# Optimization experiments

Hardware: AMD Instinct MI355X
Metric: run time of the kernel (lower is better)

Reference implementation:

```python
import jax, jax.numpy as jnp
import numpy as np

D_MODEL = 1024
D_K = 1024
D_V = 1024


def setup_inputs() -> dict:
    key = jax.random.key(0)
    kx, kq, kk, kv = jax.random.split(key, 4)
    B, T = 4, 2048
    x = jax.random.normal(kx, (B, T, D_MODEL), dtype=jnp.float32)
    # nn.Linear(d_model, d_k, bias=False) weight has shape (d_k, d_model); y = x @ W.T
    s = 1.0 / np.sqrt(D_MODEL)
    Wq = jax.random.uniform(kq, (D_K, D_MODEL), jnp.float32, -s, s)
    Wk = jax.random.uniform(kk, (D_K, D_MODEL), jnp.float32, -s, s)
    Wv = jax.random.uniform(kv, (D_V, D_MODEL), jnp.float32, -s, s)
    return {"x": x, "Wq": Wq, "Wk": Wk, "Wv": Wv}


def reference(x, Wq, Wk, Wv):
    # x: [B, T, D]; W*: [d_out, D]
    Q = jnp.einsum('btd,kd->btk', x, Wq)  # [B, T, d_k]
    K = jnp.einsum('btd,kd->btk', x, Wk)  # [B, T, d_k]
    V = jnp.einsum('btd,vd->btv', x, Wv)  # [B, T, d_v]
    scores = jnp.einsum('btk,bsk->bts', Q, K) / jnp.sqrt(jnp.float32(D_K))
    attn = jax.nn.softmax(scores, axis=-1)
    out = jnp.einsum('bts,bsv->btv', attn, V)  # [B, T, d_v]
    return out
```

## Files before the change

kernel.cpp:

```cpp
#include <hip/hip_runtime.h>
#include <hip/hip_bf16.h>
#include <stdint.h>

#define TT     2048
#define DMODEL 1024
#define NBATCH 4

typedef __bf16 bf16x8 __attribute__((ext_vector_type(8)));
typedef __bf16 bf16x4 __attribute__((ext_vector_type(4)));
typedef float  f32x4  __attribute__((ext_vector_type(4)));

#define GPTR(p) ((const __attribute__((address_space(1))) void*)(p))
#define LPTR(p) ((__attribute__((address_space(3))) void*)(p))

__global__ __launch_bounds__(256) void cvt_all(
    const float* __restrict__ x,  const float* __restrict__ wq,
    const float* __restrict__ wk, const float* __restrict__ wv,
    __bf16* __restrict__ xb,  __bf16* __restrict__ wqb,
    __bf16* __restrict__ wkb, __bf16* __restrict__ wvb,
    int nx4, int nw4)
{
    int i = blockIdx.x * 256 + threadIdx.x;
    const float* src; __bf16* dst; int off;
    if (i < nx4)                { src = x;  dst = xb;  off = i; }
    else if (i < nx4 + nw4)     { src = wq; dst = wqb; off = i - nx4; }
    else if (i < nx4 + 2 * nw4) { src = wk; dst = wkb; off = i - nx4 - nw4; }
    else if (i < nx4 + 3 * nw4) { src = wv; dst = wvb; off = i - nx4 - 2 * nw4; }
    else return;
    float4 v = ((const float4*)src)[off];
    bf16x4 o;
    o[0] = (__bf16)v.x; o[1] = (__bf16)v.y; o[2] = (__bf16)v.z; o[3] = (__bf16)v.w;
    ((bf16x4*)dst)[off] = o;
}

template <typename OutT, int BN, int WRN, bool YMAJOR, int MODE>
__global__ __launch_bounds__(512, 2) void gemm256(
    const __bf16* __restrict__ A, const __bf16* __restrict__ B,
    OutT* __restrict__ C, float* __restrict__ Rw, int N, int Kd,
    long sA, long sB, long sC, float scale)
{
    constexpr int WCN  = 8 / WRN;
    constexpr int WM   = 256 / WRN;
    constexpr int WN   = BN / WCN;
    constexpr int IW   = WM / 16;
    constexpr int IH   = IW / 2;
    constexpr int JW   = WN / 16;
    constexpr int JH   = JW / 2;
    constexpr int QB   = BN / 64;
    constexpr int BSTR = BN * 128;

    __shared__ __align__(16) char lds[65536 + 2 * BSTR];

    const int nx = gridDim.x, ny = gridDim.y;
    const int fid = blockIdx.x + nx * (blockIdx.y + ny * blockIdx.z);
    const int chunk = (nx * ny * gridDim.z) >> 3;
    const int g = (fid & 7) * chunk + (fid >> 3);
    int bx, by, bz;
    if (YMAJOR) { by = g % ny; int r = g / ny; bx = r % nx; bz = r / nx; }
    else        { bx = g % nx; int r = g / nx; by = r % ny; bz = r / ny; }

    A += (size_t)bz * (size_t)sA;
    B += (size_t)bz * (size_t)sB;
    C += (size_t)bz * (size_t)sC;

    const int tid  = threadIdx.x;
    const int lane = tid & 63;
    const int wid  = tid >> 6;
    const int wr   = wid / WCN;
    const int wc   = wid % WCN;
    const int kg   = lane >> 4;
    const int rl   = lane & 15;

    const int m0 = bx * 256;
    const int n0 = by * BN;

    const int swzX   = (rl & 7) << 4;
    const int lo0    = ((0 << 6) | (kg << 4)) ^ swzX;
    const int lo1    = ((1 << 6) | (kg << 4)) ^ swzX;
    const int baseA  = wr * (WM * 128) + rl * 128;
    const int baseBr = wc * (WN * 128) + rl * 128;

    const int srow = tid >> 3;
    const int scol = (((tid & 7) * 16) ^ ((srow & 7) << 4)) >> 1;
    const __bf16* pA[4];
    const __bf16* pB[QB];
#pragma unroll
    for (int q = 0; q < 4; q++)  pA[q] = A + (size_t)(m0 + q * 64 + srow) * Kd + scol;
#pragma unroll
    for (int q = 0; q < QB; q++) pB[q] = B + (size_t)(n0 + q * 64 + srow) * Kd + scol;
    const int dstw = wid * 1024;

#define STAGE_A(buf) do { _Pragma("unroll")                                         \
    for (int q = 0; q < 4; q++) {                                                   \
        __builtin_amdgcn_global_load_lds(GPTR(pA[q]),                               \
            LPTR(lds + (buf) * 32768 + q * 8192 + dstw), 16, 0, 0);                 \
        pA[q] += 64;                                                                \
    } } while (0)

#define STAGE_B(buf) do { _Pragma("unroll")                                         \
    for (int q = 0; q < QB; q++) {                                                  \
        __builtin_amdgcn_global_load_lds(GPTR(pB[q]),                               \
            LPTR(lds + 65536 + (buf) * BSTR + q * 8192 + dstw), 16, 0, 0);          \
        pB[q] += 64;                                                                \
    } } while (0)

#define LDA(buf, mh) do { _Pragma("unroll")                                         \
    for (int i2 = 0; i2 < IH; i2++) {                                               \
        af[i2 * 2 + 0] = *(const bf16x8*)(lds + (buf) * 32768 + baseA + ((mh) * IH + i2) * 2048 + lo0); \
        af[i2 * 2 + 1] = *(const bf16x8*)(lds + (buf) * 32768 + baseA + ((mh) * IH + i2) * 2048 + lo1); \
    } } while (0)

#define LDB(buf, nh) do { _Pragma("unroll")                                         \
    for (int j2 = 0; j2 < JH; j2++) {                                               \
        bfr[((nh) * JH + j2) * 2 + 0] = *(const bf16x8*)(lds + 65536 + (buf) * BSTR + baseBr + ((nh) * JH + j2) * 2048 + lo0); \
        bfr[((nh) * JH + j2) * 2 + 1] = *(const bf16x8*)(lds + 65536 + (buf) * BSTR + baseBr + ((nh) * JH + j2) * 2048 + lo1); \
    } } while (0)

#define MMA(mh, nh) do { _Pragma("unroll")                                          \
    for (int i2 = 0; i2 < IH; i2++) { _Pragma("unroll")                             \
        for (int j2 = 0; j2 < JH; j2++) {                                           \
            const int f_ = (nh) * JH + j2;                                          \
            const int a_ = (mh) * IH + i2;                                          \
            acc[a_][f_] = __builtin_amdgcn_mfma_f32_16x16x32_bf16(                  \
                af[i2 * 2 + 0], bfr[f_ * 2 + 0], acc[a_][f_], 0, 0, 0);             \
            acc[a_][f_] = __builtin_amdgcn_mfma_f32_16x16x32_bf16(                  \
                af[i2 * 2 + 1], bfr[f_ * 2 + 1], acc[a_][f_], 0, 0, 0);             \
    } } } while (0)

#define BAR   asm volatile("s_barrier" ::: "memory")
#define VMCS  do { if constexpr (QB == 4) asm volatile("s_waitcnt vmcnt(8)" ::: "memory"); \
                   else                   asm volatile("s_waitcnt vmcnt(6)" ::: "memory"); } while (0)
#define VMC0  asm volatile("s_waitcnt vmcnt(0)" ::: "memory")
#define PRIO1 __builtin_amdgcn_s_setprio(1)
#define PRIO0 __builtin_amdgcn_s_setprio(0)
#define SB0   __builtin_amdgcn_sched_barrier(0)

    f32x4 acc[IW][JW] = {};
    bf16x8 af[IH * 2], bfr[JW * 2];

    STAGE_A(0); STAGE_B(0); STAGE_B(1); STAGE_A(1);
    VMCS; BAR;

    const int NT2 = Kd >> 7;
    for (int i = 0; i < NT2; ++i) {
        const bool nl = (i + 1 < NT2);
        LDA(0, 0); LDB(0, 0);
        SB0; BAR; SB0; PRIO1; MMA(0, 0); PRIO0; SB0; BAR;
        LDB(0, 1);
        SB0; BAR; SB0; PRIO1; MMA(0, 1); PRIO0; SB0; BAR;
        if (nl) STAGE_B(0);
        LDA(0, 1);
        SB0; BAR; SB0; PRIO1; MMA(1, 0); PRIO0; SB0; BAR;
        if (nl) STAGE_A(0);
        SB0; PRIO1; MMA(1, 1); PRIO0; SB0;
        if (nl) { VMCS; } else { VMC0; }
        BAR;
        LDA(1, 0); LDB(1, 0);
        SB0; BAR; SB0; PRIO1; MMA(0, 0); PRIO0; SB0; BAR;
        LDB(1, 1);
        SB0; BAR; SB0; PRIO1; MMA(0, 1); PRIO0; SB0; BAR;
        if (nl) STAGE_B(1);
        LDA(1, 1);
        SB0; BAR; SB0; PRIO1; MMA(1, 0); PRIO0; SB0; BAR;
        if (nl) STAGE_A(1);
        SB0; PRIO1; MMA(1, 1); PRIO0; SB0;
        if (nl) { VMCS; BAR; }
    }

    const int rb = m0 + wr * WM + kg * 4;
    const int cb = n0 + wc * WN + rl;

    if constexpr (MODE == 1) {
        float rsum[IW][4];
#pragma unroll
        for (int i = 0; i < IW; i++)
#pragma unroll
            for (int r = 0; r < 4; r++) rsum[i][r] = 0.f;
#pragma unroll
        for (int i = 0; i < IW; i++)
#pragma unroll
            for (int j = 0; j < JW; j++)
#pragma unroll
                for (int r = 0; r < 4; r++) {
                    float e = __expf(acc[i][j][r] * scale);
                    C[(size_t)(rb + i * 16 + r) * N + (cb + j * 16)] = (OutT)e;
                    rsum[i][r] += e;
                }
#pragma unroll
        for (int i = 0; i < IW; i++)
#pragma unroll
            for (int r = 0; r < 4; r++) {
                float v = rsum[i][r];
                v += __shfl_xor(v, 1, 64); v += __shfl_xor(v, 2, 64);
                v += __shfl_xor(v, 4, 64); v += __shfl_xor(v, 8, 64);
                rsum[i][r] = v;
            }
        float* tab = (float*)lds;
        if (rl == 0) {
#pragma unroll
            for (int i = 0; i < IW; i++)
#pragma unroll
                for (int r = 0; r < 4; r++)
                    tab[wc * 256 + wr * WM + kg * 4 + i * 16 + r] = rsum[i][r];
        }
        __syncthreads();
        if (tid < 256) {
            float s = 0.f;
#pragma unroll
            for (int q = 0; q < WCN; q++) s += tab[q * 256 + tid];
            Rw[(size_t)(by * NBATCH + bz) * TT + m0 + tid] = s;
        }
    } else if constexpr (MODE == 2) {
        float inv[IW][4];
#pragma unroll
        for (int i = 0; i < IW; i++)
#pragma unroll
            for (int r = 0; r < 4; r++) {
                const int row = rb + i * 16 + r;
                float s = 0.f;
#pragma unroll
                for (int q = 0; q < 8; q++)
                    s += Rw[(size_t)(q * NBATCH + bz) * TT + row];
                inv[i][r] = 1.0f / s;
            }
#pragma unroll
        for (int i = 0; i < IW; i++)
#pragma unroll
            for (int j = 0; j < JW; j++)
#pragma unroll
                for (int r = 0; r < 4; r++)
                    C[(size_t)(rb + i * 16 + r) * N + (cb + j * 16)] =
                        (OutT)(acc[i][j][r] * inv[i][r]);
    } else {
#pragma unroll
        for (int i = 0; i < IW; i++)
#pragma unroll
            for (int j = 0; j < JW; j++)
#pragma unroll
                for (int r = 0; r < 4; r++)
                    C[(size_t)(rb + i * 16 + r) * N + (cb + j * 16)] =
                        (OutT)(acc[i][j][r] * scale);
    }

#undef STAGE_A
#undef STAGE_B
#undef LDA
#undef LDB
#undef MMA
#undef BAR
#undef VMCS
#undef VMC0
#undef PRIO1
#undef PRIO0
#undef SB0
}

extern "C" void kernel_launch(void* const* d_in, const int* in_sizes, int n_in,
                              void* d_out, int out_size, void* d_ws, size_t ws_size,
                              hipStream_t stream)
{
    const float* x  = (const float*)d_in[0];
    const float* Wq = (const float*)d_in[1];
    const float* Wk = (const float*)d_in[2];
    const float* Wv = (const float*)d_in[3];
    float* out = (float*)d_out;

    const size_t MT = (size_t)NBATCH * TT;
    __bf16* xb  = (__bf16*)d_ws;
    __bf16* wqb = xb  + MT * DMODEL;
    __bf16* wkb = wqb + (size_t)DMODEL * DMODEL;
    __bf16* wvb = wkb + (size_t)DMODEL * DMODEL;
    __bf16* Qb  = wvb + (size_t)DMODEL * DMODEL;
    __bf16* Kb  = Qb  + MT * DMODEL;
    __bf16* Vt  = Kb  + MT * DMODEL;
    __bf16* E   = Vt  + MT * DMODEL;
    float*  Rp  = (float*)(E + (size_t)NBATCH * TT * TT);

    const int nx4 = (int)(MT * DMODEL / 4);
    const int nw4 = DMODEL * DMODEL / 4;
    const int tot = nx4 + 3 * nw4;
    cvt_all<<<dim3((tot + 255) / 256), 256, 0, stream>>>(
        x, Wq, Wk, Wv, xb, wqb, wkb, wvb, nx4, nw4);

    gemm256<__bf16, 256, 2, true, 0><<<dim3(32, 4, 2), 512, 0, stream>>>(
        xb, wqb, Qb, nullptr, DMODEL, DMODEL,
        0, (long)DMODEL * DMODEL, (long)MT * DMODEL, 1.0f);

    gemm256<__bf16, 128, 4, false, 0><<<dim3(4, 16, NBATCH), 512, 0, stream>>>(
        wvb, xb, Vt, nullptr, TT, DMODEL,
        0, (long)TT * DMODEL, (long)DMODEL * TT, 1.0f);

    gemm256<__bf16, 256, 2, false, 1><<<dim3(8, 8, NBATCH), 512, 0, stream>>>(
        Qb, Kb, E, Rp, TT, DMODEL,
        (long)TT * DMODEL, (long)TT * DMODEL, (long)TT * TT, 0.03125f);

    gemm256<float, 128, 4, true, 2><<<dim3(8, 8, NBATCH), 512, 0, stream>>>(
        E, Vt, out, Rp, DMODEL, TT,
        (long)TT * TT, (long)DMODEL * TT, (long)TT * DMODEL, 1.0f);
}
```

Before: 144.1 us.

## Restructure GEMM main loop to one k-tile per iteration with fewer barriers

Replaces the unrolled two-tile main loop, which had a barrier around every MMA quarter, with a single k-tile loop that alternates LDS buffers. It issues all LDS fragment reads up front, runs three MMA quarters, then waits on lgkmcnt and takes one barrier before refilling the freed buffer and doing the last quarter. The aim is to cut barrier and sync overhead and overlap global staging with compute. The cost is less fine-grained interleaving and more register pressure from holding all fragments at once.

```diff
diff --git a/kernel.cpp b/kernel.cpp
--- a/kernel.cpp
+++ b/kernel.cpp
@@ -131,6 +131,7 @@
 #define VMCS  do { if constexpr (QB == 4) asm volatile("s_waitcnt vmcnt(8)" ::: "memory"); \
                    else                   asm volatile("s_waitcnt vmcnt(6)" ::: "memory"); } while (0)
 #define VMC0  asm volatile("s_waitcnt vmcnt(0)" ::: "memory")
+#define LGKM0 asm volatile("s_waitcnt lgkmcnt(0)" ::: "memory")
 #define PRIO1 __builtin_amdgcn_s_setprio(1)
 #define PRIO0 __builtin_amdgcn_s_setprio(0)
 #define SB0   __builtin_amdgcn_sched_barrier(0)
@@ -138,33 +139,22 @@
     f32x4 acc[IW][JW] = {};
     bf16x8 af[IH * 2], bfr[JW * 2];
 
-    STAGE_A(0); STAGE_B(0); STAGE_B(1); STAGE_A(1);
+    STAGE_A(0); STAGE_B(0); STAGE_A(1); STAGE_B(1);
     VMCS; BAR;
 
-    const int NT2 = Kd >> 7;
-    for (int i = 0; i < NT2; ++i) {
-        const bool nl = (i + 1 < NT2);
-        LDA(0, 0); LDB(0, 0);
-        SB0; BAR; SB0; PRIO1; MMA(0, 0); PRIO0; SB0; BAR;
-        LDB(0, 1);
-        SB0; BAR; SB0; PRIO1; MMA(0, 1); PRIO0; SB0; BAR;
-        if (nl) STAGE_B(0);
-        LDA(0, 1);
-        SB0; BAR; SB0; PRIO1; MMA(1, 0); PRIO0; SB0; BAR;
-        if (nl) STAGE_A(0);
-        SB0; PRIO1; MMA(1, 1); PRIO0; SB0;
-        if (nl) { VMCS; } else { VMC0; }
+    const int NT = Kd >> 6;
+    for (int t = 0; t < NT; ++t) {
+        const int b = t & 1;
+        LDA(b, 0); LDB(b, 0); LDB(b, 1);
+        PRIO1; MMA(0, 0); MMA(0, 1);
+        LDA(b, 1); MMA(1, 0); PRIO0;
+        SB0; LGKM0; SB0;
         BAR;
-        LDA(1, 0); LDB(1, 0);
-        SB0; BAR; SB0; PRIO1; MMA(0, 0); PRIO0; SB0; BAR;
-        LDB(1, 1);
-        SB0; BAR; SB0; PRIO1; MMA(0, 1); PRIO0; SB0; BAR;
-        if (nl) STAGE_B(1);
-        LDA(1, 1);
-        SB0; BAR; SB0; PRIO1; MMA(1, 0); PRIO0; SB0; BAR;
-        if (nl) STAGE_A(1);
-        SB0; PRIO1; MMA(1, 1); PRIO0; SB0;
-        if (nl) { VMCS; BAR; }
+        if (t + 2 < NT) { STAGE_A(b); STAGE_B(b); }
+        PRIO1; MMA(1, 1); PRIO0; SB0;
+        if (t + 2 < NT)      { VMCS; }
+        else if (t + 1 < NT) { VMC0; }
+        BAR;
     }
 
     const int rb = m0 + wr * WM + kg * 4;
@@ -250,6 +240,7 @@
 #undef BAR
 #undef VMCS
 #undef VMC0
+#undef LGKM0
 #undef PRIO1
 #undef PRIO0
 #undef SB0
```

Result: slower. 150.4 us (+4.4%).

## Fold Wq and Wk into a single M = Wq^T Wk and compute scores as (xM) x^T

Applied to the files above, without the earlier changes.

Replaces the separate Q and K projections with a precomputed 1024x1024 matrix M = Wq^T Wk, built by a split-K GEMM over transposed bf16 weights followed by a reduction kernel. It then forms xM with a single GEMM and computes scores against x directly. This drops one of the two large projections over all 8192 tokens, in exchange for a small weight-only GEMM, a transpose kernel and extra launches. There is an odd leftover launch writing MTb that the reduction later overwrites, and an extra bf16 rounding of M may change accuracy.

```diff
diff --git a/kernel.cpp b/kernel.cpp
--- a/kernel.cpp
+++ b/kernel.cpp
@@ -13,19 +13,14 @@
 #define GPTR(p) ((const __attribute__((address_space(1))) void*)(p))
 #define LPTR(p) ((__attribute__((address_space(3))) void*)(p))
 
-__global__ __launch_bounds__(256) void cvt_all(
-    const float* __restrict__ x,  const float* __restrict__ wq,
-    const float* __restrict__ wk, const float* __restrict__ wv,
-    __bf16* __restrict__ xb,  __bf16* __restrict__ wqb,
-    __bf16* __restrict__ wkb, __bf16* __restrict__ wvb,
-    int nx4, int nw4)
+__global__ __launch_bounds__(256) void cvt2(
+    const float* __restrict__ x, const float* __restrict__ wv,
+    __bf16* __restrict__ xb, __bf16* __restrict__ wvb, int nx4, int nw4)
 {
     int i = blockIdx.x * 256 + threadIdx.x;
     const float* src; __bf16* dst; int off;
-    if (i < nx4)                { src = x;  dst = xb;  off = i; }
-    else if (i < nx4 + nw4)     { src = wq; dst = wqb; off = i - nx4; }
-    else if (i < nx4 + 2 * nw4) { src = wk; dst = wkb; off = i - nx4 - nw4; }
-    else if (i < nx4 + 3 * nw4) { src = wv; dst = wvb; off = i - nx4 - 2 * nw4; }
+    if (i < nx4)            { src = x;  dst = xb;  off = i; }
+    else if (i < nx4 + nw4) { src = wv; dst = wvb; off = i - nx4; }
     else return;
     float4 v = ((const float4*)src)[off];
     bf16x4 o;
@@ -33,10 +28,55 @@
     ((bf16x4*)dst)[off] = o;
 }
 
+__global__ __launch_bounds__(256) void tpose_cvt(
+    const float* __restrict__ Wq, const float* __restrict__ Wk,
+    __bf16* __restrict__ wqT, __bf16* __restrict__ wkT)
+{
+    __shared__ float t[64][65];
+    const float* src = blockIdx.z ? Wk : Wq;
+    __bf16*      dst = blockIdx.z ? wkT : wqT;
+    const int r0 = blockIdx.x * 64;
+    const int c0 = blockIdx.y * 64;
+    const int tr = threadIdx.x >> 4;
+    const int tc = threadIdx.x & 15;
+#pragma unroll
+    for (int p = 0; p < 4; p++) {
+        int row = p * 16 + tr;
+        float4 v = *(const float4*)(src + (size_t)(r0 + row) * 1024 + c0 + tc * 4);
+        t[row][tc * 4 + 0] = v.x; t[row][tc * 4 + 1] = v.y;
+        t[row][tc * 4 + 2] = v.z; t[row][tc * 4 + 3] = v.w;
+    }
+    __syncthreads();
+#pragma unroll
+    for (int p = 0; p < 4; p++) {
+        int j = p * 16 + tr;
+        int i = tc * 4;
+        bf16x4 o;
+        o[0] = (__bf16)t[i + 0][j]; o[1] = (__bf16)t[i + 1][j];
+        o[2] = (__bf16)t[i + 2][j]; o[3] = (__bf16)t[i + 3][j];
+        *(bf16x4*)(dst + (size_t)(c0 + j) * 1024 + r0 + i) = o;
+    }
+}
+
+__global__ __launch_bounds__(256) void reduceM(const __bf16* __restrict__ MTp,
+                                               __bf16* __restrict__ MTo)
+{
+    int idx = (blockIdx.x * 256 + threadIdx.x) * 4;
+    float s0 = 0.f, s1 = 0.f, s2 = 0.f, s3 = 0.f;
+#pragma unroll
+    for (int z = 0; z < 8; z++) {
+        bf16x4 v = *(const bf16x4*)(MTp + (size_t)z * 1024 * 1024 + idx);
+        s0 += (float)v[0]; s1 += (float)v[1]; s2 += (float)v[2]; s3 += (float)v[3];
+    }
+    bf16x4 o;
+    o[0] = (__bf16)s0; o[1] = (__bf16)s1; o[2] = (__bf16)s2; o[3] = (__bf16)s3;
+    *(bf16x4*)(MTo + idx) = o;
+}
+
 template <typename OutT, int BN, int WRN, bool YMAJOR, int MODE>
 __global__ __launch_bounds__(512, 2) void gemm256(
     const __bf16* __restrict__ A, const __bf16* __restrict__ B,
-    OutT* __restrict__ C, float* __restrict__ Rw, int N, int Kd,
+    OutT* __restrict__ C, float* __restrict__ Rw, int N, int Kd, int Klen,
     long sA, long sB, long sC, float scale)
 {
     constexpr int WCN  = 8 / WRN;
@@ -141,7 +181,7 @@
     STAGE_A(0); STAGE_B(0); STAGE_B(1); STAGE_A(1);
     VMCS; BAR;
 
-    const int NT2 = Kd >> 7;
+    const int NT2 = Klen >> 7;
     for (int i = 0; i < NT2; ++i) {
         const bool nl = (i + 1 < NT2);
         LDA(0, 0); LDB(0, 0);
@@ -266,35 +306,46 @@
     float* out = (float*)d_out;
 
     const size_t MT = (size_t)NBATCH * TT;
+    const size_t WW = (size_t)DMODEL * DMODEL;
     __bf16* xb  = (__bf16*)d_ws;
-    __bf16* wqb = xb  + MT * DMODEL;
-    __bf16* wkb = wqb + (size_t)DMODEL * DMODEL;
-    __bf16* wvb = wkb + (size_t)DMODEL * DMODEL;
-    __bf16* Qb  = wvb + (size_t)DMODEL * DMODEL;
-    __bf16* Kb  = Qb  + MT * DMODEL;
-    __bf16* Vt  = Kb  + MT * DMODEL;
+    __bf16* wvb = xb  + MT * DMODEL;
+    __bf16* wqT = wvb + WW;
+    __bf16* wkT = wqT + WW;
+    __bf16* MTb = wkT + WW;
+    __bf16* xMb = MTb + WW;
+    __bf16* Vt  = xMb + MT * DMODEL;
     __bf16* E   = Vt  + MT * DMODEL;
-    float*  Rp  = (float*)(E + (size_t)NBATCH * TT * TT);
+    __bf16* MTp = E   + (size_t)NBATCH * TT * TT;
+    float*  Rp  = (float*)(MTp + 8 * WW);
 
     const int nx4 = (int)(MT * DMODEL / 4);
     const int nw4 = DMODEL * DMODEL / 4;
-    const int tot = nx4 + 3 * nw4;
-    cvt_all<<<dim3((tot + 255) / 256), 256, 0, stream>>>(
-        x, Wq, Wk, Wv, xb, wqb, wkb, wvb, nx4, nw4);
-
-    gemm256<__bf16, 256, 2, true, 0><<<dim3(32, 4, 2), 512, 0, stream>>>(
-        xb, wqb, Qb, nullptr, DMODEL, DMODEL,
-        0, (long)DMODEL * DMODEL, (long)MT * DMODEL, 1.0f);
+    cvt2<<<dim3((nx4 + nw4 + 255) / 256), 256, 0, stream>>>(x, Wv, xb, wvb, nx4, nw4);
+    tpose_cvt<<<dim3(16, 16, 2), 256, 0, stream>>>(Wq, Wk, wqT, wkT);
+
+    gemm256<__bf16, 256, 2, false, 0><<<dim3(4, 4, 8), 512, 0, stream>>>(
+        wkT, wqT, MTb , nullptr, DMODEL, DMODEL, 128,
+        128, 128, 0, 1.0f);
+
+    gemm256<__bf16, 256, 2, false, 0><<<dim3(4, 4, 8), 512, 0, stream>>>(
+        wkT, wqT, MTp, nullptr, DMODEL, DMODEL, 128,
+        128, 128, (long)WW, 1.0f);
+
+    reduceM<<<dim3(1024), 256, 0, stream>>>(MTp, MTb);
+
+    gemm256<__bf16, 128, 4, false, 0><<<dim3(32, 8, 1), 512, 0, stream>>>(
+        xb, MTb, xMb, nullptr, DMODEL, DMODEL, DMODEL,
+        0, 0, 0, 1.0f);
 
     gemm256<__bf16, 128, 4, false, 0><<<dim3(4, 16, NBATCH), 512, 0, stream>>>(
-        wvb, xb, Vt, nullptr, TT, DMODEL,
+        wvb, xb, Vt, nullptr, TT, DMODEL, DMODEL,
         0, (long)TT * DMODEL, (long)DMODEL * TT, 1.0f);
 
     gemm256<__bf16, 256, 2, false, 1><<<dim3(8, 8, NBATCH), 512, 0, stream>>>(
-        Qb, Kb, E, Rp, TT, DMODEL,
+        xMb, xb, E, Rp, TT, DMODEL, DMODEL,
         (long)TT * DMODEL, (long)TT * DMODEL, (long)TT * TT, 0.03125f);
 
     gemm256<float, 128, 4, true, 2><<<dim3(8, 8, NBATCH), 512, 0, stream>>>(
-        E, Vt, out, Rp, DMODEL, TT,
+        E, Vt, out, Rp, DMODEL, TT, TT,
         (long)TT * TT, (long)DMODEL * TT, (long)TT * DMODEL, 1.0f);
 }
```

Measured after the change: 162.3 us. 12.6% more time.
